# Kernel tuning notes

Hardware: AMD Instinct MI355X
Metric: run time of the kernel (lower is better)

Reference implementation:

```python
import jax, jax.numpy as jnp
import numpy as np

N = 150000   # total nodes across batch
E = 2400000  # edges (avg degree 16)
F = 20       # netlsd feature dim
H = 32       # hidden_channels
G = 1000     # graphs in batch
K = 30       # sort-pool k
D_TOT = H * 3 + 1  # 97, concat latent dim


def setup_inputs() -> dict:
    key = jax.random.key(0)
    ks = jax.random.split(key, 20)
    s = lambda fan: 1.0 / np.sqrt(fan)
    inp = {
        "x": jax.random.normal(ks[0], (N, F), jnp.float32),
        "edge_index": jax.random.randint(ks[1], (2, E), 0, N),
        "batch": jnp.sort(jax.random.randint(ks[2], (N,), 0, G)),
        # GCN conv params: (20->32), (32->32), (32->32), (32->1)
        "W0": jax.random.normal(ks[3], (F, H), jnp.float32) * s(F),
        "b0": jnp.zeros((H,), jnp.float32),
        "W1": jax.random.normal(ks[4], (H, H), jnp.float32) * s(H),
        "b1": jnp.zeros((H,), jnp.float32),
        "W2": jax.random.normal(ks[5], (H, H), jnp.float32) * s(H),
        "b2": jnp.zeros((H,), jnp.float32),
        "W3": jax.random.normal(ks[6], (H, 1), jnp.float32) * s(H),
        "b3": jnp.zeros((1,), jnp.float32),
        # conv1d head: Conv1d(1,16,97,stride=97), Conv1d(16,32,5,stride=1)
        "conv1_w": jax.random.normal(ks[7], (16, 1, D_TOT), jnp.float32) * s(D_TOT),
        "conv1_b": jnp.zeros((16,), jnp.float32),
        "conv2_w": jax.random.normal(ks[8], (32, 16, 5), jnp.float32) * s(16 * 5),
        "conv2_b": jnp.zeros((32,), jnp.float32),
        # MLP([352, 32, 1]) (dropout inactive at inference)
        "mlp_w1": jax.random.normal(ks[9], (352, 32), jnp.float32) * s(352),
        "mlp_b1": jnp.zeros((32,), jnp.float32),
        "mlp_w2": jax.random.normal(ks[10], (32, 1), jnp.float32) * s(32),
        "mlp_b2": jnp.zeros((1,), jnp.float32),
    }
    return inp


def reference(x, edge_index, batch, W0, b0, W1, b1, W2, b2, W3, b3,
              conv1_w, conv1_b, conv2_w, conv2_b,
              mlp_w1, mlp_b1, mlp_w2, mlp_b2):
    n = x.shape[0]
    # add self-loops (GCNConv default)
    loop = jnp.arange(n)
    src = jnp.concatenate([edge_index[0], loop])
    dst = jnp.concatenate([edge_index[1], loop])
    deg = jax.ops.segment_sum(jnp.ones_like(src, x.dtype), dst, num_segments=n)
    dis = jax.lax.rsqrt(jnp.maximum(deg, 1.0))  # deg >= 1 with self-loops
    norm = dis[src] * dis[dst]  # [E+N]

    def gcn(h, W, b):
        m = (h @ W)[src] * norm[:, None]                      # gather + scale
        return jax.ops.segment_sum(m, dst, num_segments=n) + b  # scatter-add

    h = x
    xs = []
    for W, b in ((W0, b0), (W1, b1), (W2, b2), (W3, b3)):
        h = jnp.tanh(gcn(h, W, b))
        xs.append(h)
    feat = jnp.concatenate(xs, axis=-1)  # [N, 97]
    d = feat.shape[-1]

    # global_sort_pool: per-graph sort by last channel (desc), top-K, zero-pad
    last = feat[:, -1]
    order = jnp.lexsort((-last, batch))  # group by graph, desc within graph
    b_s = batch[order]
    f_s = feat[order]
    counts = jax.ops.segment_sum(jnp.ones_like(batch), batch, num_segments=G)
    starts = jnp.cumsum(counts) - counts  # exclusive prefix
    rank = jnp.arange(n) - starts[b_s]
    valid = rank < K
    pooled = jnp.zeros((G, K, d), feat.dtype).at[
        b_s, jnp.where(valid, rank, 0)
    ].add(jnp.where(valid[:, None], f_s, 0.0))  # [G, K, 97]

    seq = pooled.reshape(G, 1, K * d)  # [G, 1, 2910]
    dn = ('NCH', 'OIH', 'NCH')
    y = jax.lax.conv_general_dilated(seq, conv1_w, (d,), 'VALID',
                                     dimension_numbers=dn) + conv1_b[None, :, None]
    y = jax.nn.relu(y)  # [G, 16, 30]
    y = jax.lax.reduce_window(y, -jnp.inf, jax.lax.max,
                              (1, 1, 2), (1, 1, 2), 'VALID')  # [G, 16, 15]
    y = jax.lax.conv_general_dilated(y, conv2_w, (1,), 'VALID',
                                     dimension_numbers=dn) + conv2_b[None, :, None]
    y = jax.nn.relu(y).reshape(G, -1)  # [G, 352]
    y = jax.nn.relu(y @ mlp_w1 + mlp_b1)
    return y @ mlp_w2 + mlp_b2  # [G, 1]
```

## Files before the change

kernel.cpp:

```cpp
#include <hip/hip_runtime.h>
#include <math.h>

constexpr int D_TOT = 97;
constexpr int K_POOL = 30;
constexpr int BSHIFT = 10;
constexpr int BSIZE  = 1 << BSHIFT;
constexpr int MAXB   = 256;

__global__ __launch_bounds__(256) void k_bcount(const int* __restrict__ dst, int E,
                                                int* __restrict__ bucketcnt, int B) {
    __shared__ int h[MAXB];
    int t = threadIdx.x;
    for (int i = t; i < MAXB; i += 256) h[i] = 0;
    __syncthreads();
    int e0 = blockIdx.x * 4096;
    int e1 = min(e0 + 4096, E);
    for (int i = e0 + t; i < e1; i += 256)
        atomicAdd(&h[dst[i] >> BSHIFT], 1);
    __syncthreads();
    for (int i = t; i < B; i += 256)
        if (h[i]) atomicAdd(&bucketcnt[i], h[i]);
}

__global__ void k_bscan(const int* __restrict__ cnt, int* __restrict__ bstart,
                        int* __restrict__ bcursor, int B, int E) {
    __shared__ int s[MAXB];
    int t = threadIdx.x;
    int mine = (t < B) ? cnt[t] : 0;
    s[t] = mine;
    __syncthreads();
    for (int off = 1; off < MAXB; off <<= 1) {
        int add = (t >= off) ? s[t - off] : 0;
        __syncthreads();
        s[t] += add;
        __syncthreads();
    }
    if (t < B) { int ex = s[t] - mine; bstart[t] = ex; bcursor[t] = ex; }
    if (t == 0) bstart[B] = E;
}

__global__ void k_starts(const int* __restrict__ batch, int n, int G,
                         int* __restrict__ starts) {
    int g = blockIdx.x * blockDim.x + threadIdx.x;
    if (g > G) return;
    if (g == G) { starts[G] = n; return; }
    int lo = 0, hi = n;
    while (lo < hi) { int mid = (lo + hi) >> 1; if (batch[mid] < g) lo = mid + 1; else hi = mid; }
    starts[g] = lo;
}

__global__ __launch_bounds__(256) void k_part(const int* __restrict__ src,
                                              const int* __restrict__ dst, int E, int B,
                                              int* __restrict__ bcursor,
                                              unsigned* __restrict__ bpk) {
    __shared__ int s_src[4096];
    __shared__ int s_dst[4096];
    __shared__ int hist[MAXB];
    __shared__ int base[MAXB];
    int t = threadIdx.x;
    int e0 = blockIdx.x * 4096;
    int cnt = min(4096, E - e0);
    for (int i = t; i < MAXB; i += 256) hist[i] = 0;
    __syncthreads();
    for (int i = t; i < cnt; i += 256) {
        int d = dst[e0 + i];
        s_src[i] = src[e0 + i];
        s_dst[i] = d;
        atomicAdd(&hist[d >> BSHIFT], 1);
    }
    __syncthreads();
    for (int i = t; i < B; i += 256) {
        int hh = hist[i];
        base[i] = hh ? atomicAdd(&bcursor[i], hh) : 0;
        hist[i] = 0;
    }
    __syncthreads();
    for (int i = t; i < cnt; i += 256) {
        int d = s_dst[i];
        int b = d >> BSHIFT;
        int off = atomicAdd(&hist[b], 1);
        bpk[base[b] + off] = ((unsigned)(d & (BSIZE - 1)) << 18) | (unsigned)s_src[i];
    }
}

__global__ __launch_bounds__(256) void k_fill3(const unsigned* __restrict__ bpk,
                                               const int* __restrict__ bstart,
                                               int n, int B,
                                               int* __restrict__ deg,
                                               int* __restrict__ rowstart,
                                               float* __restrict__ dis,
                                               int* __restrict__ ssrc) {
    __shared__ int cnt[BSIZE];
    __shared__ int s256[256];
    int b = blockIdx.x;
    int t = threadIdx.x;
    int s0 = bstart[b], s1 = bstart[b + 1];

    for (int i = t; i < BSIZE; i += 256) cnt[i] = 0;
    __syncthreads();
    for (int i = s0 + t; i < s1; i += 256)
        atomicAdd(&cnt[bpk[i] >> 18], 1);
    __syncthreads();

    int c0 = cnt[4 * t], c1 = cnt[4 * t + 1], c2 = cnt[4 * t + 2], c3 = cnt[4 * t + 3];
    int tot = c0 + c1 + c2 + c3;
    s256[t] = tot;
    __syncthreads();
    for (int off = 1; off < 256; off <<= 1) {
        int add = (t >= off) ? s256[t - off] : 0;
        __syncthreads();
        s256[t] += add;
        __syncthreads();
    }
    int g0 = s0 + s256[t] - tot;
    int p0 = g0, p1 = g0 + c0, p2 = p1 + c1, p3 = p2 + c2;

    int node0 = (b << BSHIFT) + 4 * t;
    if (node0 + 0 < n) { rowstart[node0 + 0] = p0; deg[node0 + 0] = c0; dis[node0 + 0] = rsqrtf((float)(c0 + 1)); }
    if (node0 + 1 < n) { rowstart[node0 + 1] = p1; deg[node0 + 1] = c1; dis[node0 + 1] = rsqrtf((float)(c1 + 1)); }
    if (node0 + 2 < n) { rowstart[node0 + 2] = p2; deg[node0 + 2] = c2; dis[node0 + 2] = rsqrtf((float)(c2 + 1)); }
    if (node0 + 3 < n) { rowstart[node0 + 3] = p3; deg[node0 + 3] = c3; dis[node0 + 3] = rsqrtf((float)(c3 + 1)); }

    cnt[4 * t] = p0; cnt[4 * t + 1] = p1; cnt[4 * t + 2] = p2; cnt[4 * t + 3] = p3;
    __syncthreads();

    for (int i = s0 + t; i < s1; i += 256) {
        unsigned pk = bpk[i];
        int pos = atomicAdd(&cnt[pk >> 18], 1);
        ssrc[pos] = (int)(pk & 0x3FFFFu);
    }
}

__global__ void k_transform0(const float* __restrict__ h,
                             const float* __restrict__ W,
                             const float* __restrict__ dis,
                             float* __restrict__ g, int n) {
    int t = blockIdx.x * blockDim.x + threadIdx.x;
    int i = t / 32, c = t % 32;
    if (i >= n) return;
    const float* hr = h + (size_t)i * 20;
    float a = 0.f;
#pragma unroll
    for (int f = 0; f < 20; ++f) a += hr[f] * W[f * 32 + c];
    g[(size_t)i * 32 + c] = dis[i] * a;
}

template<int MODE>
__global__ __launch_bounds__(256) void k_gather32f(
    const int* __restrict__ rowstart, const int* __restrict__ deg,
    const int* __restrict__ ssrc, const float4* __restrict__ g4,
    const float* __restrict__ dis, const float* __restrict__ bias,
    const float* __restrict__ Wn,
    float* __restrict__ feat, int off,
    float* __restrict__ gnext, int n)
{
    __shared__ float hs[32][33];
    __shared__ float wsm[32 * 32];
    int t = blockIdx.x * 256 + threadIdx.x;
    int i = t >> 3, p = t & 7;
    bool valid = (i < n);

    if (MODE == 0) {
        for (int q = threadIdx.x; q < 1024; q += 256) wsm[q] = Wn[q];
    }

    float h0 = 0.f, h1 = 0.f, h2 = 0.f, h3 = 0.f;
    float sc = 0.f;
    if (valid) {
        int r0 = rowstart[i], d = deg[i];
        float4 acc = g4[(size_t)i * 8 + p];
        int j = 0;
        for (; j + 4 <= d; j += 4) {
            int s0 = ssrc[r0 + j + 0];
            int s1 = ssrc[r0 + j + 1];
            int s2 = ssrc[r0 + j + 2];
            int s3 = ssrc[r0 + j + 3];
            float4 v0 = g4[(size_t)s0 * 8 + p];
            float4 v1 = g4[(size_t)s1 * 8 + p];
            float4 v2 = g4[(size_t)s2 * 8 + p];
            float4 v3 = g4[(size_t)s3 * 8 + p];
            acc.x += (v0.x + v1.x) + (v2.x + v3.x);
            acc.y += (v0.y + v1.y) + (v2.y + v3.y);
            acc.z += (v0.z + v1.z) + (v2.z + v3.z);
            acc.w += (v0.w + v1.w) + (v2.w + v3.w);
        }
        for (; j < d; ++j) {
            int s = ssrc[r0 + j];
            float4 v = g4[(size_t)s * 8 + p];
            acc.x += v.x; acc.y += v.y; acc.z += v.z; acc.w += v.w;
        }
        sc = dis[i];
        h0 = tanhf(sc * acc.x + bias[p * 4 + 0]);
        h1 = tanhf(sc * acc.y + bias[p * 4 + 1]);
        h2 = tanhf(sc * acc.z + bias[p * 4 + 2]);
        h3 = tanhf(sc * acc.w + bias[p * 4 + 3]);
        float* fr = feat + (size_t)i * D_TOT + off + p * 4;
        fr[0] = h0; fr[1] = h1; fr[2] = h2; fr[3] = h3;
    }

    int nl = threadIdx.x >> 3;
    hs[nl][p * 4 + 0] = h0;
    hs[nl][p * 4 + 1] = h1;
    hs[nl][p * 4 + 2] = h2;
    hs[nl][p * 4 + 3] = h3;
    __syncthreads();

    if (MODE == 0) {
        if (valid) {
            float a0 = 0.f, a1 = 0.f, a2 = 0.f, a3 = 0.f;
            const float* hr = hs[nl];
            int c0 = p * 4;
#pragma unroll
            for (int f = 0; f < 32; ++f) {
                float hv = hr[f];
                const float* wr = &wsm[f * 32 + c0];
                a0 += hv * wr[0];
                a1 += hv * wr[1];
                a2 += hv * wr[2];
                a3 += hv * wr[3];
            }
            float4* gn = (float4*)gnext;
            gn[(size_t)i * 8 + p] = make_float4(sc * a0, sc * a1, sc * a2, sc * a3);
        }
    } else {
        if (valid && p == 0) {
            float a = 0.f;
            const float* hr = hs[nl];
#pragma unroll
            for (int f = 0; f < 32; ++f) a += hr[f] * Wn[f];
            gnext[i] = sc * a;
        }
    }
}

__global__ void k_gather1(const int* __restrict__ rowstart, const int* __restrict__ deg,
                          const int* __restrict__ ssrc, const float* __restrict__ g,
                          const float* __restrict__ dis, const float* __restrict__ b,
                          float* __restrict__ feat, int off, int n) {
    int i = blockIdx.x * blockDim.x + threadIdx.x;
    if (i >= n) return;
    int r0 = rowstart[i], d = deg[i];
    float acc = g[i];
    for (int j = 0; j < d; ++j) acc += g[ssrc[r0 + j]];
    feat[(size_t)i * D_TOT + off] = tanhf(dis[i] * acc + b[0]);
}

constexpr int SORTN = 512;

__global__ __launch_bounds__(256) void k_cnn(
    const float* __restrict__ feat,
    const int* __restrict__ starts,
    const float* __restrict__ c1w, const float* __restrict__ c1b,
    const float* __restrict__ c2w, const float* __restrict__ c2b,
    const float* __restrict__ m1w, const float* __restrict__ m1b,
    const float* __restrict__ m2w, const float* __restrict__ m2b,
    float* __restrict__ out)
{
    int g = blockIdx.x;
    int tid = threadIdx.x;

    __shared__ unsigned long long keys[SORTN];
    __shared__ float pooled[K_POOL][D_TOT];
    __shared__ float y[16][K_POOL];
    __shared__ float z[16][15];
    __shared__ float u[352];
    __shared__ float pm[256];
    __shared__ float hid[32];

    int start = starts[g];
    int cnt = starts[g + 1] - start;
    if (cnt > SORTN) cnt = SORTN;
    int kk = cnt < K_POOL ? cnt : K_POOL;

    for (int i = tid; i < SORTN; i += 256) {
        unsigned long long kv;
        if (i < cnt) {
            float v = feat[(size_t)(start + i) * D_TOT + (D_TOT - 1)];
            unsigned uo = __float_as_uint(v);
            uo ^= (unsigned)((int)uo >> 31) | 0x80000000u;
            kv = ((unsigned long long)(~uo) << 32) | (unsigned)i;
        } else {
            kv = 0xFFFFFFFFFFFFFFFFull;
        }
        keys[i] = kv;
    }
    __syncthreads();

    for (int sz = 2; sz <= SORTN; sz <<= 1) {
        for (int j = sz >> 1; j > 0; j >>= 1) {
            for (int q = tid; q < SORTN; q += 256) {
                int l = q ^ j;
                if (l > q) {
                    bool asc = ((q & sz) == 0);
                    unsigned long long a = keys[q], bb = keys[l];
                    if ((a > bb) == asc) { keys[q] = bb; keys[l] = a; }
                }
            }
            __syncthreads();
        }
    }

    float* pf = &pooled[0][0];
    for (int t = tid; t < K_POOL * D_TOT; t += 256) pf[t] = 0.f;
    __syncthreads();
    for (int t = tid; t < kk * D_TOT; t += 256) {
        int r = t / D_TOT, c = t - r * D_TOT;
        int idx = (int)(keys[r] & 0xFFFFFFFFull);
        pf[t] = feat[(size_t)(start + idx) * D_TOT + c];
    }
    __syncthreads();

    for (int t = tid; t < 16 * K_POOL; t += 256) {
        int o = t / K_POOL, p = t - o * K_POOL;
        float a = c1b[o];
        const float* w = c1w + o * D_TOT;
        const float* pr = &pooled[p][0];
#pragma unroll 1
        for (int c = 0; c < D_TOT; ++c) a += pr[c] * w[c];
        y[o][p] = fmaxf(a, 0.f);
    }
    __syncthreads();

    for (int t = tid; t < 16 * 15; t += 256) {
        int o = t / 15, p = t - o * 15;
        z[o][p] = fmaxf(y[o][2 * p], y[o][2 * p + 1]);
    }
    __syncthreads();

    for (int t = tid; t < 32 * 11; t += 256) {
        int q = t / 11, p = t - q * 11;
        float a = c2b[q];
        const float* w = c2w + q * 16 * 5;
#pragma unroll 1
        for (int c = 0; c < 16; ++c) {
#pragma unroll
            for (int j = 0; j < 5; ++j) a += z[c][p + j] * w[c * 5 + j];
        }
        u[t] = fmaxf(a, 0.f);
    }
    __syncthreads();

    {
        int grp = tid >> 5, o = tid & 31;
        float a = 0.f;
        int i0 = grp * 44;
#pragma unroll 1
        for (int i = i0; i < i0 + 44; ++i) a += u[i] * m1w[i * 32 + o];
        pm[tid] = a;
    }
    __syncthreads();
    if (tid < 32) {
        float a = m1b[tid];
#pragma unroll
        for (int gg = 0; gg < 8; ++gg) a += pm[tid + 32 * gg];
        hid[tid] = fmaxf(a, 0.f);
    }
    __syncthreads();

    if (tid == 0) {
        float a = m2b[0];
#pragma unroll
        for (int m = 0; m < 32; ++m) a += hid[m] * m2w[m];
        out[g] = a;
    }
}

extern "C" void kernel_launch(void* const* d_in, const int* in_sizes, int n_in,
                              void* d_out, int out_size, void* d_ws, size_t ws_size,
                              hipStream_t stream) {
    const float* x    = (const float*)d_in[0];
    const int*   ei   = (const int*)d_in[1];
    const int*   batch= (const int*)d_in[2];
    const float* W0   = (const float*)d_in[3];
    const float* b0   = (const float*)d_in[4];
    const float* W1   = (const float*)d_in[5];
    const float* b1   = (const float*)d_in[6];
    const float* W2   = (const float*)d_in[7];
    const float* b2   = (const float*)d_in[8];
    const float* W3   = (const float*)d_in[9];
    const float* b3   = (const float*)d_in[10];
    const float* c1w  = (const float*)d_in[11];
    const float* c1b  = (const float*)d_in[12];
    const float* c2w  = (const float*)d_in[13];
    const float* c2b  = (const float*)d_in[14];
    const float* m1w  = (const float*)d_in[15];
    const float* m1b  = (const float*)d_in[16];
    const float* m2w  = (const float*)d_in[17];
    const float* m2b  = (const float*)d_in[18];

    const int n = in_sizes[0] / 20;
    const int E = in_sizes[1] / 2;
    const int G = out_size;
    const int* srcv = ei;
    const int* dstv = ei + E;
    const int B = (n + BSIZE - 1) >> BSHIFT;
    const int nE4 = (E + 4095) / 4096;

    char* ws = (char*)d_ws;
    float* feat    = (float*)ws;  ws += (size_t)n * D_TOT * sizeof(float);
    float* gA      = (float*)ws;  ws += (size_t)n * 32 * sizeof(float);
    float* gB      = (float*)ws;  ws += (size_t)n * 32 * sizeof(float);
    int*   ssrc    = (int*)ws;    ws += (size_t)E * sizeof(int);
    unsigned* bpk  = (unsigned*)ws; ws += (size_t)E * sizeof(unsigned);
    int*   rowstart= (int*)ws;    ws += (size_t)n * sizeof(int);
    int*   deg     = (int*)ws;    ws += (size_t)n * sizeof(int);
    float* dis     = (float*)ws;  ws += (size_t)n * sizeof(float);
    int*   startsb = (int*)ws;    ws += (size_t)(G + 1) * sizeof(int);
    int*   bucketcnt=(int*)ws;    ws += (size_t)MAXB * sizeof(int);
    int*   bstart  = (int*)ws;    ws += (size_t)(MAXB + 1) * sizeof(int);
    int*   bcursor = (int*)ws;    ws += (size_t)MAXB * sizeof(int);
    float* g1      = (float*)bpk;

    hipMemsetAsync(bucketcnt, 0, (size_t)MAXB * sizeof(int), stream);

    k_bcount<<<nE4, 256, 0, stream>>>(dstv, E, bucketcnt, B);
    k_bscan<<<1, MAXB, 0, stream>>>(bucketcnt, bstart, bcursor, B, E);
    k_part<<<nE4, 256, 0, stream>>>(srcv, dstv, E, B, bcursor, bpk);
    k_fill3<<<B, 256, 0, stream>>>(bpk, bstart, n, B, deg, rowstart, dis, ssrc);

    k_starts<<<(G + 256) / 256, 256, 0, stream>>>(batch, n, G, startsb);

    const int nt32 = n * 32;
    const int nb8  = (n * 8 + 255) / 256;
    k_transform0<<<(nt32 + 255) / 256, 256, 0, stream>>>(x, W0, dis, gA, n);
    k_gather32f<0><<<nb8, 256, 0, stream>>>(rowstart, deg, ssrc, (const float4*)gA, dis, b0, W1, feat, 0, gB, n);
    k_gather32f<0><<<nb8, 256, 0, stream>>>(rowstart, deg, ssrc, (const float4*)gB, dis, b1, W2, feat, 32, gA, n);
    k_gather32f<1><<<nb8, 256, 0, stream>>>(rowstart, deg, ssrc, (const float4*)gA, dis, b2, W3, feat, 64, g1, n);
    k_gather1<<<(n + 255) / 256, 256, 0, stream>>>(rowstart, deg, ssrc, g1, dis, b3, feat, 96, n);

    k_cnn<<<G, 256, 0, stream>>>(feat, startsb,
                                 c1w, c1b, c2w, c2b, m1w, m1b, m2w, m2b,
                                 (float*)d_out);
}
```

Baseline: 481.9 us.

## Fuse small kernels: scan+starts, fill+transform0, last-layer gather into CNN

```diff
diff --git a/kernel.cpp b/kernel.cpp
--- a/kernel.cpp
+++ b/kernel.cpp
@@ -14,59 +14,88 @@
     for (int i = t; i < MAXB; i += 256) h[i] = 0;
     __syncthreads();
     int e0 = blockIdx.x * 4096;
-    int e1 = min(e0 + 4096, E);
-    for (int i = e0 + t; i < e1; i += 256)
-        atomicAdd(&h[dst[i] >> BSHIFT], 1);
+    int cnt = min(4096, E - e0);
+    if (cnt == 4096) {
+        const int4* d4 = (const int4*)(dst + e0);
+        for (int i = t; i < 1024; i += 256) {
+            int4 v = d4[i];
+            atomicAdd(&h[v.x >> BSHIFT], 1);
+            atomicAdd(&h[v.y >> BSHIFT], 1);
+            atomicAdd(&h[v.z >> BSHIFT], 1);
+            atomicAdd(&h[v.w >> BSHIFT], 1);
+        }
+    } else {
+        for (int i = t; i < cnt; i += 256)
+            atomicAdd(&h[dst[e0 + i] >> BSHIFT], 1);
+    }
     __syncthreads();
     for (int i = t; i < B; i += 256)
         if (h[i]) atomicAdd(&bucketcnt[i], h[i]);
 }
 
-__global__ void k_bscan(const int* __restrict__ cnt, int* __restrict__ bstart,
-                        int* __restrict__ bcursor, int B, int E) {
-    __shared__ int s[MAXB];
+__global__ void k_bscan_starts(const int* __restrict__ cnt, int* __restrict__ bstart,
+                               int* __restrict__ bcursor, int B, int E,
+                               const int* __restrict__ batch, int n, int G,
+                               int* __restrict__ starts) {
     int t = threadIdx.x;
-    int mine = (t < B) ? cnt[t] : 0;
-    s[t] = mine;
-    __syncthreads();
-    for (int off = 1; off < MAXB; off <<= 1) {
-        int add = (t >= off) ? s[t - off] : 0;
+    if (blockIdx.x == 0) {
+        __shared__ int s[MAXB];
+        int mine = (t < B) ? cnt[t] : 0;
+        s[t] = mine;
         __syncthreads();
-        s[t] += add;
-        __syncthreads();
-    }
-    if (t < B) { int ex = s[t] - mine; bstart[t] = ex; bcursor[t] = ex; }
-    if (t == 0) bstart[B] = E;
-}
-
-__global__ void k_starts(const int* __restrict__ batch, int n, int G,
-                         int* __restrict__ starts) {
-    int g = blockIdx.x * blockDim.x + threadIdx.x;
-    if (g > G) return;
-    if (g == G) { starts[G] = n; return; }
-    int lo = 0, hi = n;
-    while (lo < hi) { int mid = (lo + hi) >> 1; if (batch[mid] < g) lo = mid + 1; else hi = mid; }
-    starts[g] = lo;
+        for (int off = 1; off < MAXB; off <<= 1) {
+            int add = (t >= off) ? s[t - off] : 0;
+            __syncthreads();
+            s[t] += add;
+            __syncthreads();
+        }
+        if (t < B) { int ex = s[t] - mine; bstart[t] = ex; bcursor[t] = ex; }
+        if (t == 0) bstart[B] = E;
+    } else {
+        int g = (blockIdx.x - 1) * 256 + t;
+        if (g > G) return;
+        if (g == G) { starts[G] = n; return; }
+        int lo = 0, hi = n;
+        while (lo < hi) { int mid = (lo + hi) >> 1; if (batch[mid] < g) lo = mid + 1; else hi = mid; }
+        starts[g] = lo;
+    }
 }
 
 __global__ __launch_bounds__(256) void k_part(const int* __restrict__ src,
                                               const int* __restrict__ dst, int E, int B,
                                               int* __restrict__ bcursor,
                                               unsigned* __restrict__ bpk) {
-    __shared__ int s_src[4096];
-    __shared__ int s_dst[4096];
+    __shared__ int4 s_src4[1024];
+    __shared__ int4 s_dst4[1024];
     __shared__ int hist[MAXB];
     __shared__ int base[MAXB];
+    int* s_src = (int*)s_src4;
+    int* s_dst = (int*)s_dst4;
     int t = threadIdx.x;
     int e0 = blockIdx.x * 4096;
     int cnt = min(4096, E - e0);
     for (int i = t; i < MAXB; i += 256) hist[i] = 0;
     __syncthreads();
-    for (int i = t; i < cnt; i += 256) {
-        int d = dst[e0 + i];
-        s_src[i] = src[e0 + i];
-        s_dst[i] = d;
-        atomicAdd(&hist[d >> BSHIFT], 1);
+    if (cnt == 4096) {
+        const int4* sv4 = (const int4*)(src + e0);
+        const int4* dv4 = (const int4*)(dst + e0);
+        for (int i = t; i < 1024; i += 256) {
+            int4 a = sv4[i];
+            int4 b = dv4[i];
+            s_src4[i] = a;
+            s_dst4[i] = b;
+            atomicAdd(&hist[b.x >> BSHIFT], 1);
+            atomicAdd(&hist[b.y >> BSHIFT], 1);
+            atomicAdd(&hist[b.z >> BSHIFT], 1);
+            atomicAdd(&hist[b.w >> BSHIFT], 1);
+        }
+    } else {
+        for (int i = t; i < cnt; i += 256) {
+            int d = dst[e0 + i];
+            s_src[i] = src[e0 + i];
+            s_dst[i] = d;
+            atomicAdd(&hist[d >> BSHIFT], 1);
+        }
     }
     __syncthreads();
     for (int i = t; i < B; i += 256) {
@@ -89,13 +118,19 @@
                                                int* __restrict__ deg,
                                                int* __restrict__ rowstart,
                                                float* __restrict__ dis,
-                                               int* __restrict__ ssrc) {
+                                               int* __restrict__ ssrc,
+                                               const float* __restrict__ x,
+                                               const float* __restrict__ W0,
+                                               float* __restrict__ gA) {
     __shared__ int cnt[BSIZE];
     __shared__ int s256[256];
+    __shared__ float w0s[20 * 32];
+    __shared__ float sdis[BSIZE];
     int b = blockIdx.x;
     int t = threadIdx.x;
     int s0 = bstart[b], s1 = bstart[b + 1];
 
+    for (int q = t; q < 640; q += 256) w0s[q] = W0[q];
     for (int i = t; i < BSIZE; i += 256) cnt[i] = 0;
     __syncthreads();
     for (int i = s0 + t; i < s1; i += 256)
@@ -115,11 +150,16 @@
     int g0 = s0 + s256[t] - tot;
     int p0 = g0, p1 = g0 + c0, p2 = p1 + c1, p3 = p2 + c2;
 
+    float d0 = rsqrtf((float)(c0 + 1)), d1 = rsqrtf((float)(c1 + 1));
+    float d2 = rsqrtf((float)(c2 + 1)), d3 = rsqrtf((float)(c3 + 1));
+    sdis[4 * t + 0] = d0; sdis[4 * t + 1] = d1;
+    sdis[4 * t + 2] = d2; sdis[4 * t + 3] = d3;
+
     int node0 = (b << BSHIFT) + 4 * t;
-    if (node0 + 0 < n) { rowstart[node0 + 0] = p0; deg[node0 + 0] = c0; dis[node0 + 0] = rsqrtf((float)(c0 + 1)); }
-    if (node0 + 1 < n) { rowstart[node0 + 1] = p1; deg[node0 + 1] = c1; dis[node0 + 1] = rsqrtf((float)(c1 + 1)); }
-    if (node0 + 2 < n) { rowstart[node0 + 2] = p2; deg[node0 + 2] = c2; dis[node0 + 2] = rsqrtf((float)(c2 + 1)); }
-    if (node0 + 3 < n) { rowstart[node0 + 3] = p3; deg[node0 + 3] = c3; dis[node0 + 3] = rsqrtf((float)(c3 + 1)); }
+    if (node0 + 0 < n) { rowstart[node0 + 0] = p0; deg[node0 + 0] = c0; dis[node0 + 0] = d0; }
+    if (node0 + 1 < n) { rowstart[node0 + 1] = p1; deg[node0 + 1] = c1; dis[node0 + 1] = d1; }
+    if (node0 + 2 < n) { rowstart[node0 + 2] = p2; deg[node0 + 2] = c2; dis[node0 + 2] = d2; }
+    if (node0 + 3 < n) { rowstart[node0 + 3] = p3; deg[node0 + 3] = c3; dis[node0 + 3] = d3; }
 
     cnt[4 * t] = p0; cnt[4 * t + 1] = p1; cnt[4 * t + 2] = p2; cnt[4 * t + 3] = p3;
     __syncthreads();
@@ -129,20 +169,17 @@
         int pos = atomicAdd(&cnt[pk >> 18], 1);
         ssrc[pos] = (int)(pk & 0x3FFFFu);
     }
-}
-
-__global__ void k_transform0(const float* __restrict__ h,
-                             const float* __restrict__ W,
-                             const float* __restrict__ dis,
-                             float* __restrict__ g, int n) {
-    int t = blockIdx.x * blockDim.x + threadIdx.x;
-    int i = t / 32, c = t % 32;
-    if (i >= n) return;
-    const float* hr = h + (size_t)i * 20;
-    float a = 0.f;
-#pragma unroll
-    for (int f = 0; f < 20; ++f) a += hr[f] * W[f * 32 + c];
-    g[(size_t)i * 32 + c] = dis[i] * a;
+
+    int basei = b << BSHIFT;
+    int nn = min(BSIZE, n - basei);
+    for (int q = t; q < nn * 32; q += 256) {
+        int il = q >> 5, c = q & 31;
+        const float* xr = x + (size_t)(basei + il) * 20;
+        float a = 0.f;
+#pragma unroll
+        for (int f = 0; f < 20; ++f) a += xr[f] * w0s[f * 32 + c];
+        gA[(size_t)(basei + il) * 32 + c] = sdis[il] * a;
+    }
 }
 
 template<int MODE>
@@ -233,23 +270,14 @@
     }
 }
 
-__global__ void k_gather1(const int* __restrict__ rowstart, const int* __restrict__ deg,
-                          const int* __restrict__ ssrc, const float* __restrict__ g,
-                          const float* __restrict__ dis, const float* __restrict__ b,
-                          float* __restrict__ feat, int off, int n) {
-    int i = blockIdx.x * blockDim.x + threadIdx.x;
-    if (i >= n) return;
-    int r0 = rowstart[i], d = deg[i];
-    float acc = g[i];
-    for (int j = 0; j < d; ++j) acc += g[ssrc[r0 + j]];
-    feat[(size_t)i * D_TOT + off] = tanhf(dis[i] * acc + b[0]);
-}
-
 constexpr int SORTN = 512;
 
 __global__ __launch_bounds__(256) void k_cnn(
     const float* __restrict__ feat,
     const int* __restrict__ starts,
+    const int* __restrict__ rowstart, const int* __restrict__ deg,
+    const int* __restrict__ ssrc, const float* __restrict__ g1,
+    const float* __restrict__ dis, const float* __restrict__ b3,
     const float* __restrict__ c1w, const float* __restrict__ c1b,
     const float* __restrict__ c2w, const float* __restrict__ c2b,
     const float* __restrict__ m1w, const float* __restrict__ m1b,
@@ -260,6 +288,7 @@
     int tid = threadIdx.x;
 
     __shared__ unsigned long long keys[SORTN];
+    __shared__ float vals[SORTN];
     __shared__ float pooled[K_POOL][D_TOT];
     __shared__ float y[16][K_POOL];
     __shared__ float z[16][15];
@@ -271,11 +300,23 @@
     int cnt = starts[g + 1] - start;
     if (cnt > SORTN) cnt = SORTN;
     int kk = cnt < K_POOL ? cnt : K_POOL;
-
-    for (int i = tid; i < SORTN; i += 256) {
+    float bias3 = b3[0];
+
+    for (int il = tid; il < cnt; il += 256) {
+        int i = start + il;
+        int r0 = rowstart[i], d = deg[i];
+        float acc = g1[i];
+        for (int j = 0; j < d; ++j) acc += g1[ssrc[r0 + j]];
+        vals[il] = tanhf(dis[i] * acc + bias3);
+    }
+    __syncthreads();
+
+    int SN = (cnt <= 256) ? 256 : SORTN;
+
+    for (int i = tid; i < SN; i += 256) {
         unsigned long long kv;
         if (i < cnt) {
-            float v = feat[(size_t)(start + i) * D_TOT + (D_TOT - 1)];
+            float v = vals[i];
             unsigned uo = __float_as_uint(v);
             uo ^= (unsigned)((int)uo >> 31) | 0x80000000u;
             kv = ((unsigned long long)(~uo) << 32) | (unsigned)i;
@@ -286,9 +327,9 @@
     }
     __syncthreads();
 
-    for (int sz = 2; sz <= SORTN; sz <<= 1) {
+    for (int sz = 2; sz <= SN; sz <<= 1) {
         for (int j = sz >> 1; j > 0; j >>= 1) {
-            for (int q = tid; q < SORTN; q += 256) {
+            for (int q = tid; q < SN; q += 256) {
                 int l = q ^ j;
                 if (l > q) {
                     bool asc = ((q & sz) == 0);
@@ -303,10 +344,14 @@
     float* pf = &pooled[0][0];
     for (int t = tid; t < K_POOL * D_TOT; t += 256) pf[t] = 0.f;
     __syncthreads();
-    for (int t = tid; t < kk * D_TOT; t += 256) {
-        int r = t / D_TOT, c = t - r * D_TOT;
+    for (int t = tid; t < kk * 96; t += 256) {
+        int r = t / 96, c = t - r * 96;
         int idx = (int)(keys[r] & 0xFFFFFFFFull);
-        pf[t] = feat[(size_t)(start + idx) * D_TOT + c];
+        pooled[r][c] = feat[(size_t)(start + idx) * D_TOT + c];
+    }
+    for (int r = tid; r < kk; r += 256) {
+        int idx = (int)(keys[r] & 0xFFFFFFFFull);
+        pooled[r][96] = vals[idx];
     }
     __syncthreads();
 
@@ -414,21 +459,19 @@
     hipMemsetAsync(bucketcnt, 0, (size_t)MAXB * sizeof(int), stream);
 
     k_bcount<<<nE4, 256, 0, stream>>>(dstv, E, bucketcnt, B);
-    k_bscan<<<1, MAXB, 0, stream>>>(bucketcnt, bstart, bcursor, B, E);
+    const int nSB = (G + 1 + 255) / 256;
+    k_bscan_starts<<<1 + nSB, 256, 0, stream>>>(bucketcnt, bstart, bcursor, B, E,
+                                                batch, n, G, startsb);
     k_part<<<nE4, 256, 0, stream>>>(srcv, dstv, E, B, bcursor, bpk);
-    k_fill3<<<B, 256, 0, stream>>>(bpk, bstart, n, B, deg, rowstart, dis, ssrc);
-
-    k_starts<<<(G + 256) / 256, 256, 0, stream>>>(batch, n, G, startsb);
-
-    const int nt32 = n * 32;
-    const int nb8  = (n * 8 + 255) / 256;
-    k_transform0<<<(nt32 + 255) / 256, 256, 0, stream>>>(x, W0, dis, gA, n);
+    k_fill3<<<B, 256, 0, stream>>>(bpk, bstart, n, B, deg, rowstart, dis, ssrc,
+                                   x, W0, gA);
+
+    const int nb8 = (n * 8 + 255) / 256;
     k_gather32f<0><<<nb8, 256, 0, stream>>>(rowstart, deg, ssrc, (const float4*)gA, dis, b0, W1, feat, 0, gB, n);
     k_gather32f<0><<<nb8, 256, 0, stream>>>(rowstart, deg, ssrc, (const float4*)gB, dis, b1, W2, feat, 32, gA, n);
     k_gather32f<1><<<nb8, 256, 0, stream>>>(rowstart, deg, ssrc, (const float4*)gA, dis, b2, W3, feat, 64, g1, n);
-    k_gather1<<<(n + 255) / 256, 256, 0, stream>>>(rowstart, deg, ssrc, g1, dis, b3, feat, 96, n);
-
-    k_cnn<<<G, 256, 0, stream>>>(feat, startsb,
+
+    k_cnn<<<G, 256, 0, stream>>>(feat, startsb, rowstart, deg, ssrc, g1, dis, b3,
                                  c1w, c1b, c2w, c2b, m1w, m1b, m2w, m2b,
                                  (float*)d_out);
 }
```

After: 482.5 us. Within noise of the previous version (+0.1%).
